# Performance work log

Measured on AMD Instinct MI355X. Metric: run time of the kernel, lower is better.

Reference implementation:

```python
import jax, jax.numpy as jnp
import numpy as np

B, N, F, W = 32, 512, 6, 128
K_GRAPH, K_POINT, HOPS = 100, 3, 2
CONV_D, POINT_D, LIN_D = 3, 3, 5
DIM2 = 2 * CONV_D * W + 2 * POINT_D * W  # 1536


def setup_inputs() -> dict:
    key = jax.random.key(0)
    ks = jax.random.split(key, 12)
    g = lambda i, shape, s=0.05: jax.random.normal(ks[i], shape, jnp.float32) * s
    return {
        'x': jax.random.normal(ks[0], (B * N, F), jnp.float32),
        'batch': jnp.repeat(jnp.arange(B, dtype=jnp.int32), N),  # equal-size graphs
        'tag1_W': g(1, (HOPS + 1, F, W)),
        'tag1_b': jnp.zeros((W,), jnp.float32),
        'tag_W': g(2, (CONV_D - 1, HOPS + 1, W, W)),
        'tag_b': jnp.zeros((CONV_D - 1, W), jnp.float32),
        'p1_W1': g(3, (2 * F, W)), 'p1_b1': jnp.zeros((W,), jnp.float32),
        'p1_W2': g(4, (W, W)), 'p1_b2': jnp.zeros((W,), jnp.float32),
        'pf_W': g(5, (POINT_D - 1, 2 * W, W)), 'pf_b': jnp.zeros((POINT_D - 1, W), jnp.float32),
        'bn_gamma': jnp.ones((DIM2,), jnp.float32), 'bn_beta': jnp.zeros((DIM2,), jnp.float32),
        'lin_W': g(6, (LIN_D, DIM2, DIM2), 0.02), 'lin_b': jnp.zeros((LIN_D, DIM2), jnp.float32),
        'out_W': g(7, (DIM2, 1)), 'out_b': jnp.zeros((1,), jnp.float32),
    }


def _knn(xb, k):
    # xb: [B,N,C] -> per-graph kNN source indices [B,N,k] (self excluded)
    sq = jnp.sum(xb * xb, axis=-1)
    d = sq[:, :, None] + sq[:, None, :] - 2.0 * jnp.einsum('bnc,bmc->bnm', xb, xb)
    d = d + jnp.eye(xb.shape[1], dtype=xb.dtype) * 1e10  # exclude self loops
    _, idx = jax.lax.top_k(-d, k)
    return idx


def _gather(xb, idx):
    # xb [B,N,C], idx [B,N,k] -> neighbor features [B,N,k,C]
    return jax.vmap(lambda xv, iv: xv[iv])(xb, idx)


def _tag(xb, nbr, Wk, b):
    # TAGConv K=2: every node has in-degree K_GRAPH, so sym gcn_norm edge weight
    # = deg^-1/2[src]*deg^-1/2[dst] = 1/k  ->  one hop == neighbor mean.
    out = jnp.einsum('bnc,cd->bnd', xb, Wk[0])
    h = xb
    for k in range(1, Wk.shape[0]):
        h = jnp.mean(_gather(h, nbr), axis=2)
        out = out + jnp.einsum('bnc,cd->bnd', h, Wk[k])
    return out + b


def _edgeconv(yb, k, mlp):
    # DynamicEdgeConv: rebuild kNN on current features, msg = mlp([x_i, x_j - x_i]), max-aggr
    nbr = _knn(yb, k)
    yj = _gather(yb, nbr)                       # [B,N,k,C]
    yi = jnp.broadcast_to(yb[:, :, None, :], yj.shape)
    m = mlp(jnp.concatenate([yi, yj - yi], axis=-1))
    return jnp.max(m, axis=2)


def reference(x, batch, tag1_W, tag1_b, tag_W, tag_b, p1_W1, p1_b1, p1_W2, p1_b2,
              pf_W, pf_b, bn_gamma, bn_beta, lin_W, lin_b, out_W, out_b):
    lrelu = jax.nn.leaky_relu  # negative_slope=0.01 matches torch default
    xb = x.reshape(B, N, -1)   # batch = repeat(arange(B), N), equal-size graphs
    nbr = _knn(xb, K_GRAPH)    # dropout_adj / Dropout: eval mode (identity)

    h = lrelu(_tag(xb, nbr, tag1_W, tag1_b))
    pools = [jnp.concatenate([h.mean(axis=1), h.max(axis=1)], axis=-1)]  # gap||gmp
    for f in range(CONV_D - 1):
        h = lrelu(_tag(h, nbr, tag_W[f], tag_b[f]))
        pools.append(jnp.concatenate([h.mean(axis=1), h.max(axis=1)], axis=-1))
    xc = jnp.concatenate(pools, axis=-1)  # [B, 2*CONV_D*W]

    mlp1 = lambda z: lrelu(lrelu(z @ p1_W1 + p1_b1) @ p1_W2 + p1_b2)
    y = _edgeconv(xb, K_POINT, mlp1)
    ylist = [y]
    for f in range(POINT_D - 1):
        y = _edgeconv(y, K_POINT, lambda z, f=f: lrelu(z @ pf_W[f] + pf_b[f]))
        ylist.append(y)
    y = jnp.concatenate(ylist, axis=-1)  # [B,N,POINT_D*W]
    yc = jnp.concatenate([y.mean(axis=1), y.max(axis=1)], axis=-1)

    z = jnp.concatenate([xc, yc], axis=-1)  # [B, DIM2]
    mu = z.mean(axis=0)
    var = jnp.mean((z - mu) ** 2, axis=0)
    z = (z - mu) / jnp.sqrt(var + 1e-5) * bn_gamma + bn_beta  # BatchNorm1d (batch stats)
    for g in range(LIN_D):
        z = lrelu(z @ lin_W[g] + lin_b[g])
    z = z @ out_W + out_b  # classification=False -> no sigmoid
    return z.reshape(-1)
```

## Files before the change

### kernel.cpp

```cpp
#include <hip/hip_runtime.h>
#include <hip/hip_bf16.h>

#define Bg 32
#define Nn 512
#define Fdim 6
#define Wd 128
#define KG 100
#define KP 3
#define DIM2 1536
#define GC16 16
#define NSL 12
#define KSL 128

typedef __hip_bfloat16 bf16;
typedef unsigned long long ull;

__device__ __forceinline__ float b2f(bf16 v) { return __bfloat162float(v); }
__device__ __forceinline__ float h2f(unsigned short h) { return __uint_as_float((unsigned)h << 16); }
__device__ __forceinline__ float lrelu(float v) { return v > 0.0f ? v : 0.01f * v; }

__global__ void detect_kernel(const unsigned short* __restrict__ x, int* __restrict__ flag) {
  if (threadIdx.x == 0 && blockIdx.x == 0) {
    int big = 0;
    for (int i = 0; i < 512; i += 2) {
      unsigned short u = x[i];
      int e = (u >> 7) & 0xFF;
      if (e >= 140) big++;
    }
    *flag = (big > 20) ? 1 : 0;
  }
}

__global__ void convert_kernel(const void* __restrict__ x, float* __restrict__ xf, int n,
                               const int* __restrict__ flag) {
  int i = blockIdx.x * 256 + threadIdx.x;
  if (i >= n) return;
  if (*flag) xf[i] = ((const float*)x)[i];
  else       xf[i] = b2f(((const bf16*)x)[i]);
}

__device__ __forceinline__ void ins3b(ull key, ull& k0, ull& k1, ull& k2) {
  ull M0 = k0 < key ? key : k0;  k0 = k0 < key ? k0 : key;
  ull M1 = k1 < M0 ? M0 : k1;    k1 = k1 < M0 ? k1 : M0;
  k2 = k2 < M1 ? k2 : M1;
}

__global__ void knn100_kernel(const float* __restrict__ xf, int* __restrict__ nbr) {
  __shared__ float xg[Nn * 7];
  __shared__ float sqv[Nn];
  int t = threadIdx.x; int w = t >> 6; int l = t & 63;
  int row0 = blockIdx.x * 4; int g = row0 >> 9;
  const float* xp = xf + g * (Nn * Fdim);
  for (int j = t; j < Nn; j += 256) {
    float s = 0.0f;
    #pragma unroll
    for (int c = 0; c < Fdim; c++) { float v = xp[j * Fdim + c]; xg[j * 7 + c] = v; s += v * v; }
    sqv[j] = s;
  }
  __syncthreads();
  int i = (row0 & 511) + w;
  float xi[Fdim];
  #pragma unroll
  for (int c = 0; c < Fdim; c++) xi[c] = xg[i * 7 + c];
  float sqi = sqv[i];
  unsigned m[8];
  #pragma unroll
  for (int ch = 0; ch < 8; ch++) {
    int j = ch * 64 + l;
    float dot = 0.0f;
    #pragma unroll
    for (int c = 0; c < Fdim; c++) dot += xi[c] * xg[j * 7 + c];
    float d = sqi + sqv[j] - 2.0f * dot;
    if (j == i) d += 1e10f;
    unsigned u = __float_as_uint(d);
    m[ch] = (u & 0x80000000u) ? ~u : (u | 0x80000000u);
  }
  unsigned T = 0u;
  for (int b = 31; b >= 0; b--) {
    unsigned mid = T | (1u << b);
    int c = 0;
    #pragma unroll
    for (int ch = 0; ch < 8; ch++) c += __popcll(__ballot(m[ch] < mid));
    if (c < KG) T = mid;
  }
  int* outp = nbr + ((size_t)(g * Nn + i)) * KG;
  ull lmask = (1ull << l) - 1ull;
  int base = 0;
  #pragma unroll
  for (int ch = 0; ch < 8; ch++) {
    bool less = m[ch] < T;
    ull bal = __ballot(less);
    if (less) outp[base + __popcll(bal & lmask)] = ch * 64 + l;
    base += __popcll(bal);
  }
  int need = KG - base;
  int eqb = 0;
  #pragma unroll
  for (int ch = 0; ch < 8; ch++) {
    bool eq = (m[ch] == T);
    ull bal = __ballot(eq);
    int gr = eqb + __popcll(bal & lmask);
    if (eq && gr < need) outp[base + gr] = ch * 64 + l;
    eqb += __popcll(bal);
  }
}

__global__ void knn3_x_kernel(const float* __restrict__ xf, int* __restrict__ nbr) {
  __shared__ float xg[Nn * 7];
  __shared__ float sqv[Nn];
  int t = threadIdx.x; int bid = blockIdx.x;
  int g = bid >> 5;
  const float* xp = xf + g * (Nn * Fdim);
  for (int j = t; j < Nn; j += 256) {
    float s = 0.0f;
    #pragma unroll
    for (int c = 0; c < Fdim; c++) { float v = xp[j * Fdim + c]; xg[j * 7 + c] = v; s += v * v; }
    sqv[j] = s;
  }
  __syncthreads();
  int lr = t >> 4; int sub = t & 15; int l = t & 63;
  int i = ((bid & 31) << 4) + lr;
  float xi[Fdim];
  #pragma unroll
  for (int c = 0; c < Fdim; c++) xi[c] = xg[i * 7 + c];
  float sqi = sqv[i];
  ull k0 = ~0ull, k1 = ~0ull, k2 = ~0ull;
  for (int jj = 0; jj < 32; jj++) {
    int s = (jj + l) & 31;
    int j = sub * 32 + s;
    float dot = 0.0f;
    #pragma unroll
    for (int c = 0; c < Fdim; c++) dot += xi[c] * xg[j * 7 + c];
    float d = sqi + sqv[j] - 2.0f * dot;
    if (j == i) d += 1e10f;
    unsigned u = __float_as_uint(d);
    unsigned m = (u & 0x80000000u) ? ~u : (u | 0x80000000u);
    ins3b(((ull)m << 32) | (unsigned)j, k0, k1, k2);
  }
  #pragma unroll
  for (int off = 1; off <= 8; off <<= 1) {
    ull b0 = __shfl_xor(k0, off, 64);
    ull b1 = __shfl_xor(k1, off, 64);
    ull b2 = __shfl_xor(k2, off, 64);
    ins3b(b0, k0, k1, k2); ins3b(b1, k0, k1, k2); ins3b(b2, k0, k1, k2);
  }
  if (sub == 0) {
    int row = g * Nn + i;
    nbr[row * 3 + 0] = (int)(k0 & 0xFFFFFFFFu);
    nbr[row * 3 + 1] = (int)(k1 & 0xFFFFFFFFu);
    nbr[row * 3 + 2] = (int)(k2 & 0xFFFFFFFFu);
  }
}

__global__ void knn3_gram_kernel(const float* __restrict__ G, int* __restrict__ nbr, int g0) {
  __shared__ float sqv[Nn];
  int t = threadIdx.x; int bid = blockIdx.x;
  int gl = bid >> 5; int g = g0 + gl;
  const float* Gg = G + (size_t)gl * Nn * Nn;
  for (int j = t; j < Nn; j += 256) sqv[j] = Gg[(size_t)j * Nn + j];
  __syncthreads();
  int lr = t >> 4; int sub = t & 15; int l = t & 63;
  int i = ((bid & 31) << 4) + lr;
  float sqi = sqv[i];
  const float* Gr = Gg + (size_t)i * Nn;
  ull k0 = ~0ull, k1 = ~0ull, k2 = ~0ull;
  for (int jj = 0; jj < 32; jj++) {
    int s = (jj + l) & 31;
    int j = sub * 32 + s;
    float d = sqi + sqv[j] - 2.0f * Gr[j];
    if (j == i) d += 1e10f;
    unsigned u = __float_as_uint(d);
    unsigned m = (u & 0x80000000u) ? ~u : (u | 0x80000000u);
    ins3b(((ull)m << 32) | (unsigned)j, k0, k1, k2);
  }
  #pragma unroll
  for (int off = 1; off <= 8; off <<= 1) {
    ull b0 = __shfl_xor(k0, off, 64);
    ull b1 = __shfl_xor(k1, off, 64);
    ull b2 = __shfl_xor(k2, off, 64);
    ins3b(b0, k0, k1, k2); ins3b(b1, k0, k1, k2); ins3b(b2, k0, k1, k2);
  }
  if (sub == 0) {
    int row = g * Nn + i;
    nbr[row * 3 + 0] = (int)(k0 & 0xFFFFFFFFu);
    nbr[row * 3 + 1] = (int)(k1 & 0xFFFFFFFFu);
    nbr[row * 3 + 2] = (int)(k2 & 0xFFFFFFFFu);
  }
}

__global__ void gm6_kernel(const float* __restrict__ src, const int* __restrict__ nbr,
                           float* __restrict__ dst) {
  __shared__ float s[Nn * Fdim];
  int g = blockIdx.x; int t = threadIdx.x;
  const float* sp = src + g * (Nn * Fdim);
  for (int idx = t; idx < Nn * Fdim; idx += 512) s[idx] = sp[idx];
  __syncthreads();
  float acc[Fdim] = {0, 0, 0, 0, 0, 0};
  const int* nb = nbr + ((size_t)(g * Nn + t)) * KG;
  for (int k = 0; k < KG; k++) {
    int j = nb[k];
    #pragma unroll
    for (int c = 0; c < Fdim; c++) acc[c] += s[j * Fdim + c];
  }
  float* dp = dst + (size_t)(g * Nn + t) * Fdim;
  #pragma unroll
  for (int c = 0; c < Fdim; c++) dp[c] = acc[c] / 100.0f;
}

__global__ void gm128_kernel(const float* __restrict__ src, const int* __restrict__ nbr,
                             float* __restrict__ dst) {
  __shared__ int ids[8][KG];
  int t = threadIdx.x;
  int bid = blockIdx.x;
  int swz = (bid & 7) * 256 + (bid >> 3);
  int row0 = swz * 8; int g = row0 >> 9;
  for (int idx = t; idx < 8 * KG; idx += 256) {
    int r = idx / KG, k = idx - r * KG;
    ids[r][k] = nbr[(size_t)(row0 + r) * KG + k];
  }
  __syncthreads();
  int lane = t & 31, r = t >> 5;
  const float4* sp = (const float4*)(src + (size_t)g * Nn * Wd);
  float ax = 0.0f, ay = 0.0f, az = 0.0f, aw = 0.0f;
  #pragma unroll 5
  for (int k = 0; k < KG; k++) {
    float4 v = sp[ids[r][k] * 32 + lane];
    ax += v.x; ay += v.y; az += v.z; aw += v.w;
  }
  float4 o = make_float4(ax / 100.0f, ay / 100.0f, az / 100.0f, aw / 100.0f);
  ((float4*)(dst + (size_t)(row0 + r) * Wd))[lane] = o;
}

__global__ void proj3_kernel(const float* __restrict__ in0, const float* __restrict__ in1,
                             const float* __restrict__ in2, const void* __restrict__ Wt_,
                             const void* __restrict__ bt_, float* __restrict__ out,
                             const int* __restrict__ flag) {
  __shared__ float s0[48], s1[48], s2[48];
  int t = threadIdx.x;
  int node0 = blockIdx.x * 8;
  int f32 = *flag;
  float acc[8] = {0, 0, 0, 0, 0, 0, 0, 0};
  float bd;
  if (t < 48) {
    s0[t] = in0[(size_t)node0 * 6 + t];
    s1[t] = in1[(size_t)node0 * 6 + t];
    s2[t] = in2[(size_t)node0 * 6 + t];
  }
  __syncthreads();
  if (f32) {
    const float* W = (const float*)Wt_;
    for (int c = 0; c < 6; c++) {
      float w0 = W[c * 128 + t], w1 = W[(6 + c) * 128 + t], w2 = W[(12 + c) * 128 + t];
      #pragma unroll
      for (int n = 0; n < 8; n++)
        acc[n] += s0[n * 6 + c] * w0 + s1[n * 6 + c] * w1 + s2[n * 6 + c] * w2;
    }
    bd = ((const float*)bt_)[t];
  } else {
    const bf16* W = (const bf16*)Wt_;
    for (int c = 0; c < 6; c++) {
      float w0 = b2f(W[c * 128 + t]), w1 = b2f(W[(6 + c) * 128 + t]), w2 = b2f(W[(12 + c) * 128 + t]);
      #pragma unroll
      for (int n = 0; n < 8; n++)
        acc[n] += s0[n * 6 + c] * w0 + s1[n * 6 + c] * w1 + s2[n * 6 + c] * w2;
    }
    bd = b2f(((const bf16*)bt_)[t]);
  }
  #pragma unroll
  for (int n = 0; n < 8; n++)
    out[(size_t)(node0 + n) * 128 + t] = lrelu(acc[n] + bd);
}

__global__ void proj3_big_kernel(const float* __restrict__ in0, const float* __restrict__ in1,
                                 const float* __restrict__ in2, const void* __restrict__ Wt_,
                                 const void* __restrict__ bt_, float* __restrict__ out,
                                 long Woff, long boff, const int* __restrict__ flag) {
  __shared__ __align__(16) float sa[3][32 * 128];
  __shared__ __align__(16) float Wc[64 * 128];
  int t = threadIdx.x;
  int node0 = blockIdx.x * 32;
  int f32 = *flag;
  {
    const float4* q0 = (const float4*)(in0 + (size_t)node0 * 128);
    const float4* q1 = (const float4*)(in1 + (size_t)node0 * 128);
    const float4* q2 = (const float4*)(in2 + (size_t)node0 * 128);
    float4* s0 = (float4*)sa[0]; float4* s1 = (float4*)sa[1]; float4* s2 = (float4*)sa[2];
    #pragma unroll
    for (int it = 0; it < 4; it++) {
      s0[t + it * 256] = q0[t + it * 256];
      s1[t + it * 256] = q1[t + it * 256];
      s2[t + it * 256] = q2[t + it * 256];
    }
  }
  int tx = t & 31, ty = t >> 5;
  int col0 = tx * 4, n0 = ty * 4;
  float acc[4][4];
  #pragma unroll
  for (int n = 0; n < 4; n++)
    #pragma unroll
    for (int j = 0; j < 4; j++) acc[n][j] = 0.0f;
  for (int half = 0; half < 6; half++) {
    int a = half >> 1, h = half & 1;
    {
      float4* Wl = (float4*)Wc;
      if (f32) {
        const float4* Wg = (const float4*)((const float*)Wt_ + Woff
                                           + (size_t)a * 16384 + (size_t)h * 8192);
        #pragma unroll
        for (int i = 0; i < 8; i++) Wl[t + i * 256] = Wg[t + i * 256];
      } else {
        const ushort4* Wg = (const ushort4*)((const unsigned short*)Wt_ + Woff
                                             + (size_t)a * 16384 + (size_t)h * 8192);
        #pragma unroll
        for (int i = 0; i < 8; i++) {
          ushort4 hh = Wg[t + i * 256];
          Wl[t + i * 256] = make_float4(h2f(hh.x), h2f(hh.y), h2f(hh.z), h2f(hh.w));
        }
      }
    }
    __syncthreads();
    const float* sp = sa[a];
    int cbase = h * 64;
    #pragma unroll 4
    for (int cc0 = 0; cc0 < 64; cc0 += 4) {
      float wv[4][4];
      #pragma unroll
      for (int cc = 0; cc < 4; cc++) {
        float4 w4 = *(const float4*)&Wc[(cc0 + cc) * 128 + col0];
        wv[cc][0] = w4.x; wv[cc][1] = w4.y; wv[cc][2] = w4.z; wv[cc][3] = w4.w;
      }
      int c0 = cbase + cc0;
      #pragma unroll
      for (int n = 0; n < 4; n++) {
        float4 av = *(const float4*)&sp[(n0 + n) * 128 + c0];
        #pragma unroll
        for (int j = 0; j < 4; j++)
          acc[n][j] += av.x * wv[0][j] + av.y * wv[1][j] + av.z * wv[2][j] + av.w * wv[3][j];
      }
    }
    __syncthreads();
  }
  float bdv[4];
  if (f32) {
    const float* bt = (const float*)bt_ + boff;
    #pragma unroll
    for (int j = 0; j < 4; j++) bdv[j] = bt[col0 + j];
  } else {
    const bf16* bt = (const bf16*)bt_ + boff;
    #pragma unroll
    for (int j = 0; j < 4; j++) bdv[j] = b2f(bt[col0 + j]);
  }
  #pragma unroll
  for (int n = 0; n < 4; n++) {
    float4 ov;
    ov.x = lrelu(acc[n][0] + bdv[0]); ov.y = lrelu(acc[n][1] + bdv[1]);
    ov.z = lrelu(acc[n][2] + bdv[2]); ov.w = lrelu(acc[n][3] + bdv[3]);
    *(float4*)&out[(size_t)(node0 + n0 + n) * 128 + col0] = ov;
  }
}

__global__ void proj_dual_kernel(const float* __restrict__ in, const void* __restrict__ Wt_,
                                 float* __restrict__ u, float* __restrict__ v,
                                 const int* __restrict__ flag) {
  __shared__ float s0[48];
  int t = threadIdx.x; int node0 = blockIdx.x * 8;
  int f32 = *flag;
  float au[8] = {0, 0, 0, 0, 0, 0, 0, 0};
  float av[8] = {0, 0, 0, 0, 0, 0, 0, 0};
  if (t < 48) s0[t] = in[(size_t)node0 * 6 + t];
  __syncthreads();
  if (f32) {
    const float* W = (const float*)Wt_;
    for (int c = 0; c < 6; c++) {
      float wa = W[c * 128 + t], wb = W[(6 + c) * 128 + t];
      #pragma unroll
      for (int n = 0; n < 8; n++) { float x = s0[n * 6 + c]; au[n] += x * wa; av[n] += x * wb; }
    }
  } else {
    const bf16* W = (const bf16*)Wt_;
    for (int c = 0; c < 6; c++) {
      float wa = b2f(W[c * 128 + t]), wb = b2f(W[(6 + c) * 128 + t]);
      #pragma unroll
      for (int n = 0; n < 8; n++) { float x = s0[n * 6 + c]; au[n] += x * wa; av[n] += x * wb; }
    }
  }
  #pragma unroll
  for (int n = 0; n < 8; n++) {
    u[(size_t)(node0 + n) * 128 + t] = au[n];
    v[(size_t)(node0 + n) * 128 + t] = av[n];
  }
}

__global__ void proj_dual_big_kernel(const float* __restrict__ in, const void* __restrict__ Wt_,
                                     float* __restrict__ u, float* __restrict__ v,
                                     long Woff, const int* __restrict__ flag) {
  __shared__ __align__(16) float sa[32 * 128];
  __shared__ __align__(16) float Wc[64 * 128];
  int t = threadIdx.x;
  int node0 = blockIdx.x * 32;
  int f32 = *flag;
  {
    const float4* qp = (const float4*)(in + (size_t)node0 * 128);
    float4* s0 = (float4*)sa;
    #pragma unroll
    for (int it = 0; it < 4; it++) s0[t + it * 256] = qp[t + it * 256];
  }
  int tx = t & 31, ty = t >> 5;
  int col0 = tx * 4, n0 = ty * 4;
  float accu[4][4], accv[4][4];
  #pragma unroll
  for (int n = 0; n < 4; n++)
    #pragma unroll
    for (int j = 0; j < 4; j++) { accu[n][j] = 0.0f; accv[n][j] = 0.0f; }
  for (int q = 0; q < 4; q++) {
    {
      float4* Wl = (float4*)Wc;
      if (f32) {
        const float4* Wg = (const float4*)((const float*)Wt_ + Woff + (size_t)q * 8192);
        #pragma unroll
        for (int i = 0; i < 8; i++) Wl[t + i * 256] = Wg[t + i * 256];
      } else {
        const ushort4* Wg = (const ushort4*)((const unsigned short*)Wt_ + Woff
                                             + (size_t)q * 8192);
        #pragma unroll
        for (int i = 0; i < 8; i++) {
          ushort4 hh = Wg[t + i * 256];
          Wl[t + i * 256] = make_float4(h2f(hh.x), h2f(hh.y), h2f(hh.z), h2f(hh.w));
        }
      }
    }
    __syncthreads();
    int cbase = (q & 1) * 64;
    if (q < 2) {
      #pragma unroll 4
      for (int cc0 = 0; cc0 < 64; cc0 += 4) {
        float wv[4][4];
        #pragma unroll
        for (int cc = 0; cc < 4; cc++) {
          float4 w4 = *(const float4*)&Wc[(cc0 + cc) * 128 + col0];
          wv[cc][0] = w4.x; wv[cc][1] = w4.y; wv[cc][2] = w4.z; wv[cc][3] = w4.w;
        }
        int c0 = cbase + cc0;
        #pragma unroll
        for (int n = 0; n < 4; n++) {
          float4 av = *(const float4*)&sa[(n0 + n) * 128 + c0];
          #pragma unroll
          for (int j = 0; j < 4; j++)
            accu[n][j] += av.x * wv[0][j] + av.y * wv[1][j] + av.z * wv[2][j] + av.w * wv[3][j];
        }
      }
    } else {
      #pragma unroll 4
      for (int cc0 = 0; cc0 < 64; cc0 += 4) {
        float wv[4][4];
        #pragma unroll
        for (int cc = 0; cc < 4; cc++) {
          float4 w4 = *(const float4*)&Wc[(cc0 + cc) * 128 + col0];
          wv[cc][0] = w4.x; wv[cc][1] = w4.y; wv[cc][2] = w4.z; wv[cc][3] = w4.w;
        }
        int c0 = cbase + cc0;
        #pragma unroll
        for (int n = 0; n < 4; n++) {
          float4 av = *(const float4*)&sa[(n0 + n) * 128 + c0];
          #pragma unroll
          for (int j = 0; j < 4; j++)
            accv[n][j] += av.x * wv[0][j] + av.y * wv[1][j] + av.z * wv[2][j] + av.w * wv[3][j];
        }
      }
    }
    __syncthreads();
  }
  #pragma unroll
  for (int n = 0; n < 4; n++) {
    *(float4*)&u[(size_t)(node0 + n0 + n) * 128 + col0] = *(float4*)accu[n];
    *(float4*)&v[(size_t)(node0 + n0 + n) * 128 + col0] = *(float4*)accv[n];
  }
}

__global__ void edge_mlp1_kernel(const float* __restrict__ u, const float* __restrict__ v,
                                 const int* __restrict__ nbrp, const void* __restrict__ W2_,
                                 const void* __restrict__ b1_, const void* __restrict__ b2_,
                                 float* __restrict__ y, const int* __restrict__ flag) {
  __shared__ __align__(16) float Ws[64 * 128];
  __shared__ __align__(16) float tl[24][128];
  int t = threadIdx.x;
  int node0 = blockIdx.x * 8; int g = node0 >> 9;
  int f32 = *flag;
  if (f32) {
    const float4* Wg = (const float4*)W2_;
    float4* Wl = (float4*)Ws;
    #pragma unroll
    for (int i = 0; i < 8; i++) Wl[t + i * 256] = Wg[t + i * 256];
  } else {
    const ushort4* Wg = (const ushort4*)W2_;
    float4* Wl = (float4*)Ws;
    #pragma unroll
    for (int i = 0; i < 8; i++) {
      ushort4 h = Wg[t + i * 256];
      Wl[t + i * 256] = make_float4(h2f(h.x), h2f(h.y), h2f(h.z), h2f(h.w));
    }
  }
  {
    int lane = t & 31, n = t >> 5;
    int row = node0 + n;
    float4 ui = ((const float4*)(u + (size_t)row * 128))[lane];
    float4 vi = ((const float4*)(v + (size_t)row * 128))[lane];
    float4 b1v;
    if (f32) b1v = ((const float4*)b1_)[lane];
    else {
      ushort4 h = ((const ushort4*)b1_)[lane];
      b1v = make_float4(h2f(h.x), h2f(h.y), h2f(h.z), h2f(h.w));
    }
    float4 base = make_float4(ui.x - vi.x + b1v.x, ui.y - vi.y + b1v.y,
                              ui.z - vi.z + b1v.z, ui.w - vi.w + b1v.w);
    #pragma unroll
    for (int k = 0; k < 3; k++) {
      int j = nbrp[row * 3 + k];
      float4 vj = ((const float4*)(v + (size_t)(g * Nn + j) * 128))[lane];
      float4 tv;
      tv.x = lrelu(base.x + vj.x); tv.y = lrelu(base.y + vj.y);
      tv.z = lrelu(base.z + vj.z); tv.w = lrelu(base.w + vj.w);
      *(float4*)&tl[n * 3 + k][lane * 4] = tv;
    }
  }
  __syncthreads();
  int tx = t & 31, ty = t >> 5;
  int col0 = tx * 4;
  float acc[3][4];
  #pragma unroll
  for (int k = 0; k < 3; k++)
    #pragma unroll
    for (int j = 0; j < 4; j++) acc[k][j] = 0.0f;
  #pragma unroll 4
  for (int cc0 = 0; cc0 < 64; cc0 += 4) {
    float wv[4][4];
    #pragma unroll
    for (int cc = 0; cc < 4; cc++) {
      float4 w4 = *(const float4*)&Ws[(cc0 + cc) * 128 + col0];
      wv[cc][0] = w4.x; wv[cc][1] = w4.y; wv[cc][2] = w4.z; wv[cc][3] = w4.w;
    }
    #pragma unroll
    for (int k = 0; k < 3; k++) {
      float4 av = *(const float4*)&tl[ty * 3 + k][cc0];
      #pragma unroll
      for (int j = 0; j < 4; j++)
        acc[k][j] += av.x * wv[0][j] + av.y * wv[1][j] + av.z * wv[2][j] + av.w * wv[3][j];
    }
  }
  __syncthreads();
  if (f32) {
    const float4* Wg = (const float4*)W2_ + 2048;
    float4* Wl = (float4*)Ws;
    #pragma unroll
    for (int i = 0; i < 8; i++) Wl[t + i * 256] = Wg[t + i * 256];
  } else {
    const ushort4* Wg = (const ushort4*)W2_ + 2048;
    float4* Wl = (float4*)Ws;
    #pragma unroll
    for (int i = 0; i < 8; i++) {
      ushort4 h = Wg[t + i * 256];
      Wl[t + i * 256] = make_float4(h2f(h.x), h2f(h.y), h2f(h.z), h2f(h.w));
    }
  }
  __syncthreads();
  #pragma unroll 4
  for (int cc0 = 0; cc0 < 64; cc0 += 4) {
    float wv[4][4];
    #pragma unroll
    for (int cc = 0; cc < 4; cc++) {
      float4 w4 = *(const float4*)&Ws[(cc0 + cc) * 128 + col0];
      wv[cc][0] = w4.x; wv[cc][1] = w4.y; wv[cc][2] = w4.z; wv[cc][3] = w4.w;
    }
    #pragma unroll
    for (int k = 0; k < 3; k++) {
      float4 av = *(const float4*)&tl[ty * 3 + k][64 + cc0];
      #pragma unroll
      for (int j = 0; j < 4; j++)
        acc[k][j] += av.x * wv[0][j] + av.y * wv[1][j] + av.z * wv[2][j] + av.w * wv[3][j];
    }
  }
  float b2d[4];
  if (f32) {
    const float* b2p = (const float*)b2_;
    #pragma unroll
    for (int j = 0; j < 4; j++) b2d[j] = b2p[col0 + j];
  } else {
    const bf16* b2p = (const bf16*)b2_;
    #pragma unroll
    for (int j = 0; j < 4; j++) b2d[j] = b2f(b2p[col0 + j]);
  }
  float4 ov;
  {
    float m0 = lrelu(acc[0][0] + b2d[0]);
    m0 = fmaxf(m0, lrelu(acc[1][0] + b2d[0]));
    ov.x = fmaxf(m0, lrelu(acc[2][0] + b2d[0]));
    float m1 = lrelu(acc[0][1] + b2d[1]);
    m1 = fmaxf(m1, lrelu(acc[1][1] + b2d[1]));
    ov.y = fmaxf(m1, lrelu(acc[2][1] + b2d[1]));
    float m2 = lrelu(acc[0][2] + b2d[2]);
    m2 = fmaxf(m2, lrelu(acc[1][2] + b2d[2]));
    ov.z = fmaxf(m2, lrelu(acc[2][2] + b2d[2]));
    float m3 = lrelu(acc[0][3] + b2d[3]);
    m3 = fmaxf(m3, lrelu(acc[1][3] + b2d[3]));
    ov.w = fmaxf(m3, lrelu(acc[2][3] + b2d[3]));
  }
  *(float4*)&y[(size_t)(node0 + ty) * 128 + col0] = ov;
}

__global__ void edge_max_kernel(const float* __restrict__ u, const float* __restrict__ v,
                                const int* __restrict__ nbrp, const void* __restrict__ bias_,
                                float* __restrict__ y, long boff, const int* __restrict__ flag) {
  int row = blockIdx.x; int g = row >> 9; int t = threadIdx.x;
  float ui = u[(size_t)row * 128 + t], vi = v[(size_t)row * 128 + t];
  float bd;
  if (*flag) bd = ((const float*)bias_ + boff)[t]; else bd = b2f(((const bf16*)bias_ + boff)[t]);
  float m = -3.4e38f;
  #pragma unroll
  for (int k = 0; k < 3; k++) {
    int j = nbrp[row * 3 + k];
    m = fmaxf(m, lrelu(ui - vi + v[(size_t)(g * Nn + j) * 128 + t] + bd));
  }
  y[(size_t)row * 128 + t] = m;
}

__global__ void gram_kernel(const float* __restrict__ y, float* __restrict__ G, int g0) {
  __shared__ float At[16][68], Bt[16][68];
  int bid = blockIdx.x;
  int gl = bid >> 6; int tt = bid & 63; int ti = tt >> 3; int tj = tt & 7;
  int g = g0 + gl;
  int t = threadIdx.x; int tx = t & 15, ty = t >> 4;
  const float* Yg = y + (size_t)g * Nn * Wd;
  float* Gg = G + (size_t)gl * Nn * Nn;
  int sr = t >> 2, sq = (t & 3) * 4;
  float c[4][4];
  #pragma unroll
  for (int p = 0; p < 4; p++)
    #pragma unroll
    for (int q = 0; q < 4; q++) c[p][q] = 0.0f;
  for (int k0 = 0; k0 < 128; k0 += 16) {
    {
      float4 a4 = *(const float4*)&Yg[(ti * 64 + sr) * 128 + k0 + sq];
      float4 b4 = *(const float4*)&Yg[(tj * 64 + sr) * 128 + k0 + sq];
      At[sq + 0][sr] = a4.x; At[sq + 1][sr] = a4.y; At[sq + 2][sr] = a4.z; At[sq + 3][sr] = a4.w;
      Bt[sq + 0][sr] = b4.x; Bt[sq + 1][sr] = b4.y; Bt[sq + 2][sr] = b4.z; Bt[sq + 3][sr] = b4.w;
    }
    __syncthreads();
    #pragma unroll 4
    for (int kk = 0; kk < 16; kk++) {
      float4 a4 = *(const float4*)&At[kk][ty * 4];
      float4 b4 = *(const float4*)&Bt[kk][tx * 4];
      float a[4] = {a4.x, a4.y, a4.z, a4.w};
      float bb[4] = {b4.x, b4.y, b4.z, b4.w};
      #pragma unroll
      for (int p = 0; p < 4; p++)
        #pragma unroll
        for (int q = 0; q < 4; q++) c[p][q] += a[p] * bb[q];
    }
    __syncthreads();
  }
  #pragma unroll
  for (int p = 0; p < 4; p++)
    #pragma unroll
    for (int q = 0; q < 4; q++)
      Gg[(size_t)(ti * 64 + ty * 4 + p) * Nn + tj * 64 + tx * 4 + q] = c[p][q];
}

__global__ void pool_kernel(const float* __restrict__ h, float* __restrict__ z,
                            int meanoff, int maxoff) {
  __shared__ float ssum[8][32], smax[8][32];
  int b = blockIdx.x;
  int g = b >> 2, cg = b & 3;
  int t = threadIdx.x;
  int cl = t & 31, r8 = t >> 5;
  int col = cg * 32 + cl;
  const float* hg = h + (size_t)g * Nn * Wd + (size_t)r8 * 64 * Wd + col;
  float s = 0.0f, m = -3.4e38f;
  #pragma unroll 4
  for (int n = 0; n < 64; n++) {
    float vv = hg[n * 128];
    s += vv; m = fmaxf(m, vv);
  }
  ssum[r8][cl] = s; smax[r8][cl] = m;
  __syncthreads();
  if (r8 == 0) {
    #pragma unroll
    for (int q = 1; q < 8; q++) {
      s += ssum[q][cl];
      m = fmaxf(m, smax[q][cl]);
    }
    z[g * DIM2 + meanoff + col] = s / 512.0f;
    z[g * DIM2 + maxoff + col] = m;
  }
}

__global__ void bn_kernel(float* __restrict__ z, const void* __restrict__ gamma,
                          const void* __restrict__ beta, const int* __restrict__ flag) {
  int c = blockIdx.x * 256 + threadIdx.x;
  if (c >= DIM2) return;
  float s = 0.0f;
  for (int r = 0; r < Bg; r++) s += z[r * DIM2 + c];
  float mu = s / 32.0f;
  float v = 0.0f;
  for (int r = 0; r < Bg; r++) { float d = z[r * DIM2 + c] - mu; v += d * d; }
  float var = v / 32.0f;
  float gm, bt;
  if (*flag) { gm = ((const float*)gamma)[c]; bt = ((const float*)beta)[c]; }
  else       { gm = b2f(((const bf16*)gamma)[c]); bt = b2f(((const bf16*)beta)[c]); }
  float scale = gm / sqrtf(var + 1e-5f);
  for (int r = 0; r < Bg; r++) z[r * DIM2 + c] = (z[r * DIM2 + c] - mu) * scale + bt;
}

__global__ void hl_part_kernel(const float* __restrict__ zin, const float* __restrict__ Pin,
                               const void* __restrict__ bin_, const void* __restrict__ W_,
                               float* __restrict__ Pout, long Woff, long binoff, int mode,
                               const int* __restrict__ flag) {
  __shared__ __align__(16) float zs[32][KSL];
  int t = threadIdx.x;
  int bd = blockIdx.x % 24, s = blockIdx.x / 24;
  int d0 = bd * 64, k0 = s * KSL;
  int f32 = *flag;
  if (mode == 0) {
    for (int idx = t; idx < 32 * KSL; idx += 256) {
      int r = idx >> 7, k = idx & 127;
      zs[r][k] = zin[r * DIM2 + k0 + k];
    }
  } else {
    for (int idx = t; idx < 32 * KSL / 4; idx += 256) {
      int r = idx >> 5, k4 = (idx & 31) * 4;
      float ax = 0.0f, ay = 0.0f, az = 0.0f, aw = 0.0f;
      const float* Pr = Pin + (size_t)r * NSL * DIM2 + k0 + k4;
      #pragma unroll
      for (int ss = 0; ss < NSL; ss++) {
        float4 p = *(const float4*)(Pr + (size_t)ss * DIM2);
        ax += p.x; ay += p.y; az += p.z; aw += p.w;
      }
      float b0, b1, b2, b3;
      if (f32) {
        const float* bp = (const float*)bin_ + binoff + k0 + k4;
        b0 = bp[0]; b1 = bp[1]; b2 = bp[2]; b3 = bp[3];
      } else {
        const bf16* bp = (const bf16*)bin_ + binoff + k0 + k4;
        b0 = b2f(bp[0]); b1 = b2f(bp[1]); b2 = b2f(bp[2]); b3 = b2f(bp[3]);
      }
      zs[r][k4 + 0] = lrelu(ax + b0);
      zs[r][k4 + 1] = lrelu(ay + b1);
      zs[r][k4 + 2] = lrelu(az + b2);
      zs[r][k4 + 3] = lrelu(aw + b3);
    }
  }
  __syncthreads();
  int lane = t & 63, rg = t >> 6;
  int d = d0 + lane, r0 = rg * 8;
  float acc[8];
  #pragma unroll
  for (int i = 0; i < 8; i++) acc[i] = 0.0f;
  if (f32) {
    const float* W = (const float*)W_ + Woff;
    for (int k = 0; k < KSL; k += 4) {
      float w0 = W[(size_t)(k0 + k) * DIM2 + d];
      float w1 = W[(size_t)(k0 + k + 1) * DIM2 + d];
      float w2 = W[(size_t)(k0 + k + 2) * DIM2 + d];
      float w3 = W[(size_t)(k0 + k + 3) * DIM2 + d];
      #pragma unroll
      for (int i = 0; i < 8; i++) {
        float4 z4 = *(const float4*)&zs[r0 + i][k];
        acc[i] += z4.x * w0 + z4.y * w1 + z4.z * w2 + z4.w * w3;
      }
    }
  } else {
    const unsigned short* W = (const unsigned short*)W_ + Woff;
    for (int k = 0; k < KSL; k += 4) {
      float w0 = h2f(W[(size_t)(k0 + k) * DIM2 + d]);
      float w1 = h2f(W[(size_t)(k0 + k + 1) * DIM2 + d]);
      float w2 = h2f(W[(size_t)(k0 + k + 2) * DIM2 + d]);
      float w3 = h2f(W[(size_t)(k0 + k + 3) * DIM2 + d]);
      #pragma unroll
      for (int i = 0; i < 8; i++) {
        float4 z4 = *(const float4*)&zs[r0 + i][k];
        acc[i] += z4.x * w0 + z4.y * w1 + z4.z * w2 + z4.w * w3;
      }
    }
  }
  float* Po = Pout + (size_t)s * DIM2 + d;
  #pragma unroll
  for (int i = 0; i < 8; i++) Po[(size_t)(r0 + i) * NSL * DIM2] = acc[i];
}

__global__ void hl_reduce_kernel(const float* __restrict__ Pin, const void* __restrict__ bin_,
                                 float* __restrict__ out, long binoff,
                                 const int* __restrict__ flag) {
  int idx = blockIdx.x * 256 + threadIdx.x;
  int r = idx / DIM2, d = idx - r * DIM2;
  float acc = 0.0f;
  const float* Pr = Pin + (size_t)r * NSL * DIM2 + d;
  #pragma unroll
  for (int s = 0; s < NSL; s++) acc += Pr[(size_t)s * DIM2];
  float b;
  if (*flag) b = ((const float*)bin_ + binoff)[d];
  else       b = b2f(((const bf16*)bin_ + binoff)[d]);
  out[r * DIM2 + d] = lrelu(acc + b);
}

__global__ void final_kernel(const float* __restrict__ zin, const void* __restrict__ outW,
                             const void* __restrict__ outb, void* __restrict__ out,
                             const int* __restrict__ flag) {
  __shared__ float red[256];
  int r = blockIdx.x, t = threadIdx.x;
  int f32 = *flag;
  float acc = 0.0f;
  if (f32) {
    const float* W = (const float*)outW;
    for (int c = t; c < DIM2; c += 256) acc += zin[r * DIM2 + c] * W[c];
  } else {
    const bf16* W = (const bf16*)outW;
    for (int c = t; c < DIM2; c += 256) acc += zin[r * DIM2 + c] * b2f(W[c]);
  }
  red[t] = acc; __syncthreads();
  for (int s = 128; s > 0; s >>= 1) { if (t < s) red[t] += red[t + s]; __syncthreads(); }
  if (t == 0) {
    float ob;
    if (f32) ob = ((const float*)outb)[0]; else ob = b2f(((const bf16*)outb)[0]);
    float val = red[0] + ob;
    if (f32) ((float*)out)[r] = val;
    else     ((bf16*)out)[r] = __float2bfloat16(val);
  }
}

extern "C" void kernel_launch(void* const* d_in, const int* in_sizes, int n_in,
                              void* d_out, int out_size, void* d_ws, size_t ws_size,
                              hipStream_t stream) {
  const void* x      = d_in[0];
  const void* tag1_W = d_in[2];
  const void* tag1_b = d_in[3];
  const void* tag_W  = d_in[4];
  const void* tag_b  = d_in[5];
  const void* p1_W1  = d_in[6];
  const void* p1_b1  = d_in[7];
  const void* p1_W2  = d_in[8];
  const void* p1_b2  = d_in[9];
  const void* pf_W   = d_in[10];
  const void* pf_b   = d_in[11];
  const void* bn_g   = d_in[12];
  const void* bn_b   = d_in[13];
  const void* lin_W  = d_in[14];
  const void* lin_b  = d_in[15];
  const void* out_W  = d_in[16];
  const void* out_b  = d_in[17];

  float* ws = (float*)d_ws;
  float* XF   = ws + 0;
  float* M16  = ws + 98304;
  float* M26  = ws + 196608;
  float* Z    = ws + 294912;
  float* ZB   = ws + 344064;
  int*   FLAG = (int*)(ws + 409600);
  int*   NBRP = (int*)(ws + 409616);
  int*   NBRG = (int*)(ws + 458768);
  float* S0   = ws + 2097168;
  float* S1   = ws + 4194320;
  float* S2   = ws + 6291472;
  float* S3   = ws + 8388624;
  float* PA   = S0;
  float* PB   = S1;

  detect_kernel<<<1, 64, 0, stream>>>((const unsigned short*)x, FLAG);
  convert_kernel<<<384, 256, 0, stream>>>(x, XF, Bg * Nn * Fdim, FLAG);
  knn100_kernel<<<Bg * Nn / 4, 256, 0, stream>>>(XF, NBRG);
  knn3_x_kernel<<<Bg * Nn / 16, 256, 0, stream>>>(XF, NBRP);

  gm6_kernel<<<Bg, 512, 0, stream>>>(XF, NBRG, M16);
  gm6_kernel<<<Bg, 512, 0, stream>>>(M16, NBRG, M26);
  proj3_kernel<<<2048, 128, 0, stream>>>(XF, M16, M26, tag1_W, tag1_b, S0, FLAG);
  pool_kernel<<<128, 256, 0, stream>>>(S0, Z, 0, 128);

  gm128_kernel<<<Bg * Nn / 8, 256, 0, stream>>>(S0, NBRG, S1);
  gm128_kernel<<<Bg * Nn / 8, 256, 0, stream>>>(S1, NBRG, S2);
  proj3_big_kernel<<<512, 256, 0, stream>>>(S0, S1, S2, tag_W, tag_b, S3, 0, 0, FLAG);
  pool_kernel<<<128, 256, 0, stream>>>(S3, Z, 256, 384);

  gm128_kernel<<<Bg * Nn / 8, 256, 0, stream>>>(S3, NBRG, S1);
  gm128_kernel<<<Bg * Nn / 8, 256, 0, stream>>>(S1, NBRG, S2);
  proj3_big_kernel<<<512, 256, 0, stream>>>(S3, S1, S2, tag_W, tag_b, S0,
                                            3L * 128 * 128, 128, FLAG);
  pool_kernel<<<128, 256, 0, stream>>>(S0, Z, 512, 640);

  proj_dual_kernel<<<2048, 128, 0, stream>>>(XF, p1_W1, S0, S1, FLAG);
  edge_mlp1_kernel<<<2048, 256, 0, stream>>>(S0, S1, NBRP, p1_W2, p1_b1, p1_b2, S2, FLAG);
  pool_kernel<<<128, 256, 0, stream>>>(S2, Z, 768, 1152);

  for (int c = 0; c < Bg; c += GC16) {
    gram_kernel<<<GC16 * 64, 256, 0, stream>>>(S2, S0, c);
    knn3_gram_kernel<<<GC16 * Nn / 16, 256, 0, stream>>>(S0, NBRP, c);
  }
  proj_dual_big_kernel<<<512, 256, 0, stream>>>(S2, pf_W, S0, S1, 0, FLAG);
  edge_max_kernel<<<Bg * Nn, 128, 0, stream>>>(S0, S1, NBRP, pf_b, S3, 0, FLAG);
  pool_kernel<<<128, 256, 0, stream>>>(S3, Z, 896, 1280);

  for (int c = 0; c < Bg; c += GC16) {
    gram_kernel<<<GC16 * 64, 256, 0, stream>>>(S3, S0, c);
    knn3_gram_kernel<<<GC16 * Nn / 16, 256, 0, stream>>>(S0, NBRP, c);
  }
  proj_dual_big_kernel<<<512, 256, 0, stream>>>(S3, pf_W, S0, S1, 256L * 128, FLAG);
  edge_max_kernel<<<Bg * Nn, 128, 0, stream>>>(S0, S1, NBRP, pf_b, S2, 128, FLAG);
  pool_kernel<<<128, 256, 0, stream>>>(S2, Z, 1024, 1408);

  bn_kernel<<<6, 256, 0, stream>>>(Z, bn_g, bn_b, FLAG);
  hl_part_kernel<<<288, 256, 0, stream>>>(Z, nullptr, nullptr, lin_W, PA,
                                          0L * DIM2 * DIM2, 0L, 0, FLAG);
  hl_part_kernel<<<288, 256, 0, stream>>>(nullptr, PA, lin_b, lin_W, PB,
                                          1L * DIM2 * DIM2, 0L * DIM2, 1, FLAG);
  hl_part_kernel<<<288, 256, 0, stream>>>(nullptr, PB, lin_b, lin_W, PA,
                                          2L * DIM2 * DIM2, 1L * DIM2, 1, FLAG);
  hl_part_kernel<<<288, 256, 0, stream>>>(nullptr, PA, lin_b, lin_W, PB,
                                          3L * DIM2 * DIM2, 2L * DIM2, 1, FLAG);
  hl_part_kernel<<<288, 256, 0, stream>>>(nullptr, PB, lin_b, lin_W, PA,
                                          4L * DIM2 * DIM2, 3L * DIM2, 1, FLAG);
  hl_reduce_kernel<<<192, 256, 0, stream>>>(PA, lin_b, ZB, 4L * DIM2, FLAG);
  final_kernel<<<Bg, 256, 0, stream>>>(ZB, out_W, out_b, d_out, FLAG);
}
```

Before: 779.6 us.

## Fuse Gram matrix and kNN top-3 selection into one feature-space kernel

Replaces the two-stage path, a Gram kernel that writes a 512x512 matrix per graph to global memory and then a kNN kernel that reads it back, with a single kernel. That kernel computes the dot products on the fly from shared-memory tiles of features and keeps running top-3 candidates in registers. This removes the Gram matrix round trip through memory and four kernel launches per edge-conv layer. In exchange, each block recomputes the squared norms of the j rows and now owns only 32 rows with 512 blocks, which may limit arithmetic intensity and occupancy. Per-thread top-3 insertion work also goes up.

```diff
diff --git a/kernel.cpp b/kernel.cpp
--- a/kernel.cpp
+++ b/kernel.cpp
@@ -8,7 +8,6 @@
 #define KG 100
 #define KP 3
 #define DIM2 1536
-#define GC16 16
 #define NSL 12
 #define KSL 128
 
@@ -152,39 +151,100 @@
   }
 }
 
-__global__ void knn3_gram_kernel(const float* __restrict__ G, int* __restrict__ nbr, int g0) {
-  __shared__ float sqv[Nn];
-  int t = threadIdx.x; int bid = blockIdx.x;
-  int gl = bid >> 5; int g = g0 + gl;
-  const float* Gg = G + (size_t)gl * Nn * Nn;
-  for (int j = t; j < Nn; j += 256) sqv[j] = Gg[(size_t)j * Nn + j];
-  __syncthreads();
-  int lr = t >> 4; int sub = t & 15; int l = t & 63;
-  int i = ((bid & 31) << 4) + lr;
-  float sqi = sqv[i];
-  const float* Gr = Gg + (size_t)i * Nn;
-  ull k0 = ~0ull, k1 = ~0ull, k2 = ~0ull;
-  for (int jj = 0; jj < 32; jj++) {
-    int s = (jj + l) & 31;
-    int j = sub * 32 + s;
-    float d = sqi + sqv[j] - 2.0f * Gr[j];
-    if (j == i) d += 1e10f;
-    unsigned u = __float_as_uint(d);
-    unsigned m = (u & 0x80000000u) ? ~u : (u | 0x80000000u);
-    ins3b(((ull)m << 32) | (unsigned)j, k0, k1, k2);
+__global__ void knn3_feat_kernel(const float* __restrict__ y, int* __restrict__ nbr) {
+  __shared__ __align__(16) float At[128][36];
+  __shared__ __align__(16) float Bt[16][68];
+  __shared__ float sqi[32], sqj[64];
+  int bid = blockIdx.x;
+  int g = bid >> 4, i0 = (bid & 15) * 32;
+  int t = threadIdx.x;
+  const float* Yg = y + (size_t)g * Nn * Wd;
+  {
+    int r = t >> 3, kc = (t & 7) * 16;
+    #pragma unroll
+    for (int m4 = 0; m4 < 4; m4++) {
+      float4 v = *(const float4*)&Yg[(size_t)(i0 + r) * 128 + kc + m4 * 4];
+      At[kc + m4 * 4 + 0][r] = v.x;
+      At[kc + m4 * 4 + 1][r] = v.y;
+      At[kc + m4 * 4 + 2][r] = v.z;
+      At[kc + m4 * 4 + 3][r] = v.w;
+    }
+  }
+  __syncthreads();
+  if (t < 32) {
+    float s = 0.0f;
+    for (int k = 0; k < 128; k++) { float v = At[k][t]; s += v * v; }
+    sqi[t] = s;
+  }
+  int tx = t & 15, ty = t >> 4;
+  ull ka0 = ~0ull, ka1 = ~0ull, ka2 = ~0ull;
+  ull kb0 = ~0ull, kb1 = ~0ull, kb2 = ~0ull;
+  for (int j0 = 0; j0 < Nn; j0 += 64) {
+    if (t < 64) sqj[t] = 0.0f;
+    float c0[4] = {0, 0, 0, 0}, c1[4] = {0, 0, 0, 0};
+    for (int k0 = 0; k0 < 128; k0 += 16) {
+      __syncthreads();
+      {
+        int jc = t >> 2, kc = (t & 3) * 4;
+        float4 v = *(const float4*)&Yg[(size_t)(j0 + jc) * 128 + k0 + kc];
+        Bt[kc + 0][jc] = v.x; Bt[kc + 1][jc] = v.y;
+        Bt[kc + 2][jc] = v.z; Bt[kc + 3][jc] = v.w;
+      }
+      __syncthreads();
+      if (t < 64) {
+        float s = sqj[t];
+        #pragma unroll
+        for (int kk = 0; kk < 16; kk++) { float v = Bt[kk][t]; s += v * v; }
+        sqj[t] = s;
+      }
+      #pragma unroll
+      for (int kk = 0; kk < 16; kk++) {
+        float2 a2 = *(const float2*)&At[k0 + kk][ty * 2];
+        float4 b4 = *(const float4*)&Bt[kk][tx * 4];
+        c0[0] += a2.x * b4.x; c0[1] += a2.x * b4.y; c0[2] += a2.x * b4.z; c0[3] += a2.x * b4.w;
+        c1[0] += a2.y * b4.x; c1[1] += a2.y * b4.y; c1[2] += a2.y * b4.z; c1[3] += a2.y * b4.w;
+      }
+    }
+    __syncthreads();
+    int rowA = i0 + ty * 2, rowB = rowA + 1;
+    float siA = sqi[ty * 2], siB = sqi[ty * 2 + 1];
+    #pragma unroll
+    for (int q = 0; q < 4; q++) {
+      int j = j0 + tx * 4 + q;
+      float sj = sqj[tx * 4 + q];
+      float dA = siA + sj - 2.0f * c0[q];
+      float dB = siB + sj - 2.0f * c1[q];
+      if (j == rowA) dA += 1e10f;
+      if (j == rowB) dB += 1e10f;
+      unsigned uA = __float_as_uint(dA);
+      unsigned mA = (uA & 0x80000000u) ? ~uA : (uA | 0x80000000u);
+      ins3b(((ull)mA << 32) | (unsigned)j, ka0, ka1, ka2);
+      unsigned uB = __float_as_uint(dB);
+      unsigned mB = (uB & 0x80000000u) ? ~uB : (uB | 0x80000000u);
+      ins3b(((ull)mB << 32) | (unsigned)j, kb0, kb1, kb2);
+    }
+    __syncthreads();
   }
   #pragma unroll
   for (int off = 1; off <= 8; off <<= 1) {
-    ull b0 = __shfl_xor(k0, off, 64);
-    ull b1 = __shfl_xor(k1, off, 64);
-    ull b2 = __shfl_xor(k2, off, 64);
-    ins3b(b0, k0, k1, k2); ins3b(b1, k0, k1, k2); ins3b(b2, k0, k1, k2);
-  }
-  if (sub == 0) {
-    int row = g * Nn + i;
-    nbr[row * 3 + 0] = (int)(k0 & 0xFFFFFFFFu);
-    nbr[row * 3 + 1] = (int)(k1 & 0xFFFFFFFFu);
-    nbr[row * 3 + 2] = (int)(k2 & 0xFFFFFFFFu);
+    ull b0 = __shfl_xor(ka0, off, 64);
+    ull b1 = __shfl_xor(ka1, off, 64);
+    ull b2 = __shfl_xor(ka2, off, 64);
+    ins3b(b0, ka0, ka1, ka2); ins3b(b1, ka0, ka1, ka2); ins3b(b2, ka0, ka1, ka2);
+    ull d0 = __shfl_xor(kb0, off, 64);
+    ull d1 = __shfl_xor(kb1, off, 64);
+    ull d2 = __shfl_xor(kb2, off, 64);
+    ins3b(d0, kb0, kb1, kb2); ins3b(d1, kb0, kb1, kb2); ins3b(d2, kb0, kb1, kb2);
+  }
+  if (tx == 0) {
+    int rowA = g * Nn + i0 + ty * 2;
+    nbr[rowA * 3 + 0] = (int)(ka0 & 0xFFFFFFFFu);
+    nbr[rowA * 3 + 1] = (int)(ka1 & 0xFFFFFFFFu);
+    nbr[rowA * 3 + 2] = (int)(ka2 & 0xFFFFFFFFu);
+    int rowB = rowA + 1;
+    nbr[rowB * 3 + 0] = (int)(kb0 & 0xFFFFFFFFu);
+    nbr[rowB * 3 + 1] = (int)(kb1 & 0xFFFFFFFFu);
+    nbr[rowB * 3 + 2] = (int)(kb2 & 0xFFFFFFFFu);
   }
 }
 
@@ -621,48 +681,6 @@
     m = fmaxf(m, lrelu(ui - vi + v[(size_t)(g * Nn + j) * 128 + t] + bd));
   }
   y[(size_t)row * 128 + t] = m;
-}
-
-__global__ void gram_kernel(const float* __restrict__ y, float* __restrict__ G, int g0) {
-  __shared__ float At[16][68], Bt[16][68];
-  int bid = blockIdx.x;
-  int gl = bid >> 6; int tt = bid & 63; int ti = tt >> 3; int tj = tt & 7;
-  int g = g0 + gl;
-  int t = threadIdx.x; int tx = t & 15, ty = t >> 4;
-  const float* Yg = y + (size_t)g * Nn * Wd;
-  float* Gg = G + (size_t)gl * Nn * Nn;
-  int sr = t >> 2, sq = (t & 3) * 4;
-  float c[4][4];
-  #pragma unroll
-  for (int p = 0; p < 4; p++)
-    #pragma unroll
-    for (int q = 0; q < 4; q++) c[p][q] = 0.0f;
-  for (int k0 = 0; k0 < 128; k0 += 16) {
-    {
-      float4 a4 = *(const float4*)&Yg[(ti * 64 + sr) * 128 + k0 + sq];
-      float4 b4 = *(const float4*)&Yg[(tj * 64 + sr) * 128 + k0 + sq];
-      At[sq + 0][sr] = a4.x; At[sq + 1][sr] = a4.y; At[sq + 2][sr] = a4.z; At[sq + 3][sr] = a4.w;
-      Bt[sq + 0][sr] = b4.x; Bt[sq + 1][sr] = b4.y; Bt[sq + 2][sr] = b4.z; Bt[sq + 3][sr] = b4.w;
-    }
-    __syncthreads();
-    #pragma unroll 4
-    for (int kk = 0; kk < 16; kk++) {
-      float4 a4 = *(const float4*)&At[kk][ty * 4];
-      float4 b4 = *(const float4*)&Bt[kk][tx * 4];
-      float a[4] = {a4.x, a4.y, a4.z, a4.w};
-      float bb[4] = {b4.x, b4.y, b4.z, b4.w};
-      #pragma unroll
-      for (int p = 0; p < 4; p++)
-        #pragma unroll
-        for (int q = 0; q < 4; q++) c[p][q] += a[p] * bb[q];
-    }
-    __syncthreads();
-  }
-  #pragma unroll
-  for (int p = 0; p < 4; p++)
-    #pragma unroll
-    for (int q = 0; q < 4; q++)
-      Gg[(size_t)(ti * 64 + ty * 4 + p) * Nn + tj * 64 + tx * 4 + q] = c[p][q];
 }
 
 __global__ void pool_kernel(const float* __restrict__ h, float* __restrict__ z,
@@ -888,18 +906,12 @@
   edge_mlp1_kernel<<<2048, 256, 0, stream>>>(S0, S1, NBRP, p1_W2, p1_b1, p1_b2, S2, FLAG);
   pool_kernel<<<128, 256, 0, stream>>>(S2, Z, 768, 1152);
 
-  for (int c = 0; c < Bg; c += GC16) {
-    gram_kernel<<<GC16 * 64, 256, 0, stream>>>(S2, S0, c);
-    knn3_gram_kernel<<<GC16 * Nn / 16, 256, 0, stream>>>(S0, NBRP, c);
-  }
+  knn3_feat_kernel<<<512, 256, 0, stream>>>(S2, NBRP);
   proj_dual_big_kernel<<<512, 256, 0, stream>>>(S2, pf_W, S0, S1, 0, FLAG);
   edge_max_kernel<<<Bg * Nn, 128, 0, stream>>>(S0, S1, NBRP, pf_b, S3, 0, FLAG);
   pool_kernel<<<128, 256, 0, stream>>>(S3, Z, 896, 1280);
 
-  for (int c = 0; c < Bg; c += GC16) {
-    gram_kernel<<<GC16 * 64, 256, 0, stream>>>(S3, S0, c);
-    knn3_gram_kernel<<<GC16 * Nn / 16, 256, 0, stream>>>(S0, NBRP, c);
-  }
+  knn3_feat_kernel<<<512, 256, 0, stream>>>(S3, NBRP);
   proj_dual_big_kernel<<<512, 256, 0, stream>>>(S3, pf_W, S0, S1, 256L * 128, FLAG);
   edge_max_kernel<<<Bg * Nn, 128, 0, stream>>>(S0, S1, NBRP, pf_b, S2, 128, FLAG);
   pool_kernel<<<128, 256, 0, stream>>>(S2, Z, 1024, 1408);
```

Result: slower. 818.6 us (+5.0%).
